# Performance work log

Measured on AMD Instinct MI355X. Metric: run time of the kernel, lower is better.

Reference implementation:

```python
import jax, jax.numpy as jnp
import numpy as np

EPS = 1e-5

def conv1x1(x, w, b):
    # x: [B,C,H,W], w: [O,C], b: [O]
    return jnp.einsum('oc,bchw->bohw', w, x) + b[None, :, None, None]

def mean_variance_norm(feat):
    # per-(batch,channel) stats over spatial dims; torch.var default is unbiased (ddof=1)
    b, c = feat.shape[:2]
    flat = feat.reshape(b, c, -1)
    mean = jnp.mean(flat, axis=2)[:, :, None, None]
    std = jnp.sqrt(jnp.var(flat, axis=2, ddof=1) + EPS)[:, :, None, None]
    return (feat - mean) / std

def setup_inputs() -> dict:
    key = jax.random.key(0)
    ks = jax.random.split(key, 10)
    B, C, H, W = 4, 256, 64, 64
    sc = 1.0 / np.sqrt(C)
    return {
        'content': jax.random.normal(ks[0], (B, C, H, W), jnp.float32),
        'style': jax.random.normal(ks[1], (B, C, H, W), jnp.float32),
        'content_key': jax.random.normal(ks[2], (B, C, H, W), jnp.float32),
        'style_key': jax.random.normal(ks[3], (B, C, H, W), jnp.float32),
        'f_w': jax.random.normal(ks[4], (C, C), jnp.float32) * sc,
        'f_b': jax.random.normal(ks[5], (C,), jnp.float32) * 0.01,
        'g_w': jax.random.normal(ks[6], (C, C), jnp.float32) * sc,
        'g_b': jax.random.normal(ks[7], (C,), jnp.float32) * 0.01,
        'h_w': jax.random.normal(ks[8], (C, C), jnp.float32) * sc,
        'h_b': jax.random.normal(ks[9], (C,), jnp.float32) * 0.01,
    }

def reference(content, style, content_key, style_key, f_w, f_b, g_w, g_b, h_w, h_b):
    Fq = conv1x1(content_key, f_w, f_b)   # [B,C,Hc,Wc]
    G = conv1x1(style_key, g_w, g_b)      # [B,C,Hs,Ws]
    Hv = conv1x1(style, h_w, h_b)         # [B,C,Hs,Ws]
    b, c, h, w = Fq.shape
    hw_c = h * w
    hw_s = G.shape[2] * G.shape[3]
    Fm = Fq.reshape(b, c, hw_c).transpose(0, 2, 1)       # [B,Nq,C]
    Gm = G.reshape(b, c, hw_s)                            # [B,C,Nk]
    style_flat = Hv.reshape(b, c, hw_s).transpose(0, 2, 1)  # [B,Nk,C]
    S = jax.nn.softmax(jnp.einsum('bqc,bck->bqk', Fm, Gm), axis=-1)  # [B,Nq,Nk]
    mean = jnp.einsum('bqk,bkc->bqc', S, style_flat)
    second = jnp.einsum('bqk,bkc->bqc', S, style_flat ** 2)
    std = jnp.sqrt(jax.nn.relu(second - mean ** 2))
    mean = mean.reshape(b, h, w, c).transpose(0, 3, 1, 2)
    std = std.reshape(b, h, w, c).transpose(0, 3, 1, 2)
    return std * mean_variance_norm(content) + mean
```

## Files before the change

kernel.cpp:

```cpp
#include <hip/hip_runtime.h>
#include <math.h>

#define NSP 4096
#define CD  256

typedef _Float16 half8 __attribute__((ext_vector_type(8)));
typedef _Float16 half4v __attribute__((ext_vector_type(4)));
typedef float f32x4 __attribute__((ext_vector_type(4)));
typedef unsigned int u32;

#define VMCNT(n) asm volatile("s_waitcnt vmcnt(" #n ")" ::: "memory")
#define LGKM0    asm volatile("s_waitcnt lgkmcnt(0)" ::: "memory")

__device__ __forceinline__ void gl16(const void* g, void* l) {
    __builtin_amdgcn_global_load_lds((const __attribute__((address_space(1))) u32*)g,
                                     (__attribute__((address_space(3))) u32*)l, 16, 0, 0);
}

template<int MODE>
__global__ __launch_bounds__(256, 2) void conv_kernel(
    const float* __restrict__ W, const float* __restrict__ bias,
    const float* __restrict__ Xall, _Float16* __restrict__ Yh, _Float16* __restrict__ Yl)
{
    const int b = blockIdx.z;
    const float* X = Xall + (size_t)b * CD * NSP;
    _Float16* Yhb = Yh + (size_t)b * CD * NSP;
    _Float16* Ylb = Yl + (size_t)b * CD * NSP;
    __shared__ float Ws[8][128];
    __shared__ float Xs[8][128];
    const int t = threadIdx.x;
    const int tx = t & 15, ty = t >> 4;
    const int m0 = blockIdx.y * 128, n0 = blockIdx.x * 128;
    float acc[8][8];
#pragma unroll
    for (int i = 0; i < 8; ++i)
#pragma unroll
        for (int j = 0; j < 8; ++j) acc[i][j] = 0.f;

    for (int k0 = 0; k0 < CD; k0 += 8) {
        __syncthreads();
        {
            int m = t >> 1, k = (t & 1) * 4;
            float4 wv = *reinterpret_cast<const float4*>(&W[(size_t)(m0 + m) * CD + k0 + k]);
            Ws[k + 0][m] = wv.x; Ws[k + 1][m] = wv.y; Ws[k + 2][m] = wv.z; Ws[k + 3][m] = wv.w;
        }
        {
            int k = t >> 5, n = (t & 31) * 4;
            *reinterpret_cast<float4*>(&Xs[k][n]) =
                *reinterpret_cast<const float4*>(&X[(size_t)(k0 + k) * NSP + n0 + n]);
        }
        __syncthreads();
#pragma unroll
        for (int k = 0; k < 8; ++k) {
            float a[8], bb[8];
            float4 a0 = *reinterpret_cast<const float4*>(&Ws[k][ty * 8]);
            float4 a1 = *reinterpret_cast<const float4*>(&Ws[k][ty * 8 + 4]);
            float4 b0 = *reinterpret_cast<const float4*>(&Xs[k][tx * 4]);
            float4 b1 = *reinterpret_cast<const float4*>(&Xs[k][64 + tx * 4]);
            a[0]=a0.x; a[1]=a0.y; a[2]=a0.z; a[3]=a0.w;
            a[4]=a1.x; a[5]=a1.y; a[6]=a1.z; a[7]=a1.w;
            bb[0]=b0.x; bb[1]=b0.y; bb[2]=b0.z; bb[3]=b0.w;
            bb[4]=b1.x; bb[5]=b1.y; bb[6]=b1.z; bb[7]=b1.w;
#pragma unroll
            for (int i = 0; i < 8; ++i)
#pragma unroll
                for (int j = 0; j < 8; ++j) acc[i][j] = fmaf(a[i], bb[j], acc[i][j]);
        }
    }
    float bv[8];
#pragma unroll
    for (int i = 0; i < 8; ++i) bv[i] = bias[m0 + ty * 8 + i];

    if (MODE == 0) {
#pragma unroll
        for (int jj = 0; jj < 8; ++jj) {
            int n = n0 + ((jj < 4) ? (tx * 4 + jj) : (64 + tx * 4 + (jj - 4)));
            half4v h0, h1, l0, l1;
#pragma unroll
            for (int i = 0; i < 4; ++i) {
                float y0 = acc[i][jj] + bv[i];
                _Float16 hh0 = (_Float16)y0; h0[i] = hh0; l0[i] = (_Float16)(y0 - (float)hh0);
                float y1 = acc[i + 4][jj] + bv[i + 4];
                _Float16 hh1 = (_Float16)y1; h1[i] = hh1; l1[i] = (_Float16)(y1 - (float)hh1);
            }
            size_t off = (size_t)n * CD + m0 + ty * 8;
            *reinterpret_cast<half4v*>(&Yhb[off])     = h0;
            *reinterpret_cast<half4v*>(&Yhb[off + 4]) = h1;
            *reinterpret_cast<half4v*>(&Ylb[off])     = l0;
            *reinterpret_cast<half4v*>(&Ylb[off + 4]) = l1;
        }
    } else if (MODE == 1) {
#pragma unroll
        for (int jj = 0; jj < 8; ++jj) {
            int n = n0 + ((jj < 4) ? (tx * 4 + jj) : (64 + tx * 4 + (jj - 4)));
            int tile = n >> 5, key = n & 31;
            int g = (m0 + ty * 8) >> 3;
            size_t base = (size_t)tile * 8192 + (size_t)key * 256
                        + ((((g * 16)) ^ ((key & 7) << 4)) >> 1);
            half4v h0, h1, l0, l1;
#pragma unroll
            for (int i = 0; i < 4; ++i) {
                float y0 = acc[i][jj] + bv[i];
                _Float16 hh0 = (_Float16)y0; h0[i] = hh0; l0[i] = (_Float16)(y0 - (float)hh0);
                float y1 = acc[i + 4][jj] + bv[i + 4];
                _Float16 hh1 = (_Float16)y1; h1[i] = hh1; l1[i] = (_Float16)(y1 - (float)hh1);
            }
            *reinterpret_cast<half4v*>(&Yhb[base])     = h0;
            *reinterpret_cast<half4v*>(&Yhb[base + 4]) = h1;
            *reinterpret_cast<half4v*>(&Ylb[base])     = l0;
            *reinterpret_cast<half4v*>(&Ylb[base + 4]) = l1;
        }
    } else {
#pragma unroll
        for (int i = 0; i < 8; ++i) {
            int ch = m0 + ty * 8 + i;
#pragma unroll
            for (int grp = 0; grp < 2; ++grp) {
                int n = n0 + grp * 64 + tx * 4;
                int tile = n >> 5, kin = n & 31;
                half4v hv, lv;
#pragma unroll
                for (int j = 0; j < 4; ++j) {
                    float y = acc[i][grp * 4 + j] + bv[i];
                    _Float16 hh = (_Float16)y; hv[j] = hh; lv[j] = (_Float16)(y - (float)hh);
                }
                size_t base = (size_t)tile * 8192 + (size_t)ch * 32
                            + ((((kin * 2)) ^ ((ch & 3) << 4)) >> 1);
                *reinterpret_cast<half4v*>(&Yhb[base]) = hv;
                *reinterpret_cast<half4v*>(&Ylb[base]) = lv;
            }
        }
    }
}

#define KB_OFF 0
#define VB_OFF 65536
#define PB_OFF 131072
#define RM_OFF 139264
#define RS_OFF 139776
#define SMEM_BYTES 140800

__global__ __launch_bounds__(512, 2) void attn_kernel(
    const _Float16* __restrict__ Qh_g, const _Float16* __restrict__ Ql_g,
    const _Float16* __restrict__ Kh_g, const _Float16* __restrict__ Kl_g,
    const _Float16* __restrict__ Vh_g, const _Float16* __restrict__ Vl_g,
    float* __restrict__ Mout, float* __restrict__ Sout)
{
    extern __shared__ char smem[];
    const int tid = threadIdx.x;
    const int lane = tid & 63;
    const int w = tid >> 6;
    const int g4 = lane >> 4;
    const int l15 = lane & 15;
    const int qf = w & 3;
    const int kf = w >> 2;

    const int bid = blockIdx.x;
    const int b = (bid & 7) >> 1;
    const int qb = ((bid >> 3) << 1) | (bid & 1);
    const int q0 = qb * 64;

    const size_t bNC = (size_t)b * NSP * CD;
    const _Float16* Qhb = Qh_g + bNC;
    const _Float16* Qlb = Ql_g + bNC;
    const _Float16* Khb = Kh_g + bNC;
    const _Float16* Klb = Kl_g + bNC;
    const _Float16* Vhb = Vh_g + bNC;
    const _Float16* Vlb = Vl_g + bNC;

    const int qrow = q0 + qf * 16 + l15;
    half8 qh[8], ql[8];
#pragma unroll
    for (int ks = 0; ks < 8; ++ks) {
        qh[ks] = *reinterpret_cast<const half8*>(Qhb + (size_t)qrow * CD + ks * 32 + g4 * 8);
        ql[ks] = *reinterpret_cast<const half8*>(Qlb + (size_t)qrow * CD + ks * 32 + g4 * 8);
    }

    auto stageK = [&](int t, int buf) {
        const _Float16* sh = Khb + (size_t)t * 8192 + w * 1024 + lane * 8;
        const _Float16* sl = Klb + (size_t)t * 8192 + w * 1024 + lane * 8;
        char* d = smem + KB_OFF + buf * 32768 + w * 2048;
        gl16(sh,       d);
        gl16(sh + 512, d + 1024);
        gl16(sl,       d + 16384);
        gl16(sl + 512, d + 16384 + 1024);
    };
    auto stageV = [&](int t, int buf) {
        const _Float16* sh = Vhb + (size_t)t * 8192 + w * 1024 + lane * 8;
        const _Float16* sl = Vlb + (size_t)t * 8192 + w * 1024 + lane * 8;
        char* d = smem + VB_OFF + buf * 32768 + w * 2048;
        gl16(sh,       d);
        gl16(sh + 512, d + 1024);
        gl16(sl,       d + 16384);
        gl16(sl + 512, d + 16384 + 1024);
    };

    stageK(0, 0); stageV(0, 0); stageK(1, 1); stageV(1, 1);

    f32x4 accM[2][4], accS[2][4];
#pragma unroll
    for (int m = 0; m < 2; ++m)
#pragma unroll
        for (int nf = 0; nf < 4; ++nf) {
            accM[m][nf] = (f32x4){0.f, 0.f, 0.f, 0.f};
            accS[m][nf] = (f32x4){0.f, 0.f, 0.f, 0.f};
        }
    float mrun = -3.0e38f, lrun = 0.f;

    const int key = kf * 16 + l15;
    const int ksw = (key & 7) << 4;

    for (int t = 0; t < 128; ++t) {
        const int buf = t & 1;

        if (t < 127) { VMCNT(12); } else { VMCNT(4); }
        LGKM0;
        __builtin_amdgcn_s_barrier();
        __builtin_amdgcn_sched_barrier(0);

        if (t > 0) {
            const float* rs = (const float*)(smem + RS_OFF + ((t + 1) & 1) * 512);
            lrun += rs[lane] + rs[64 + lane];
        }

        const char* krow = smem + KB_OFF + buf * 32768 + key * 512;
        f32x4 s = (f32x4){0.f, 0.f, 0.f, 0.f};
        __builtin_amdgcn_s_setprio(1);
#pragma unroll
        for (int ks = 0; ks < 8; ++ks) {
            int off = ((ks * 4 + g4) * 16) ^ ksw;
            half8 bh = *reinterpret_cast<const half8*>(krow + off);
            half8 bl = *reinterpret_cast<const half8*>(krow + 16384 + off);
            s = __builtin_amdgcn_mfma_f32_16x16x32_f16(qh[ks], bh, s, 0, 0, 0);
            s = __builtin_amdgcn_mfma_f32_16x16x32_f16(qh[ks], bl, s, 0, 0, 0);
            s = __builtin_amdgcn_mfma_f32_16x16x32_f16(ql[ks], bh, s, 0, 0, 0);
        }
        __builtin_amdgcn_s_setprio(0);

        f32x4 rmax = s;
#pragma unroll
        for (int mk = 1; mk <= 8; mk <<= 1)
#pragma unroll
            for (int e = 0; e < 4; ++e) rmax[e] = fmaxf(rmax[e], __shfl_xor(rmax[e], mk));
        if (l15 == 0)
            *reinterpret_cast<f32x4*>(smem + RM_OFF + kf * 256 + (qf * 16 + g4 * 4) * 4) = rmax;

        LGKM0;
        __builtin_amdgcn_s_barrier();
        __builtin_amdgcn_sched_barrier(0);

        if (t + 2 < 128) stageK(t + 2, buf);

        const float* rmf = (const float*)(smem + RM_OFF);
        float rm01 = fmaxf(rmf[lane], rmf[64 + lane]);
        bool upd = rm01 > mrun + 6.f;
        float sc = upd ? __expf(mrun - rm01) : 1.f;
        if (upd) mrun = rm01;
        lrun *= sc;

        float psum[4];
#pragma unroll
        for (int e = 0; e < 4; ++e) {
            int q_e = qf * 16 + g4 * 4 + e;
            float m_e = __shfl(mrun, q_e);
            float p = __expf(s[e] - m_e);
            _Float16 hp = (_Float16)p;
            *reinterpret_cast<_Float16*>(smem + PB_OFF + q_e * 128 + ((key * 2) ^ ((q_e & 7) << 4))) = hp;
            psum[e] = (float)hp;
        }
#pragma unroll
        for (int mk = 1; mk <= 8; mk <<= 1)
#pragma unroll
            for (int e = 0; e < 4; ++e) psum[e] += __shfl_xor(psum[e], mk);
        if (l15 == 0) {
            f32x4 ps4 = {psum[0], psum[1], psum[2], psum[3]};
            *reinterpret_cast<f32x4*>(smem + RS_OFF + buf * 512 + kf * 256 + (qf * 16 + g4 * 4) * 4) = ps4;
        }

        if (__ballot(sc < 1.f)) {
#pragma unroll
            for (int nf = 0; nf < 4; ++nf) {
                float scn = __shfl(sc, nf * 16 + l15);
#pragma unroll
                for (int m = 0; m < 2; ++m)
#pragma unroll
                    for (int e = 0; e < 4; ++e) { accM[m][nf][e] *= scn; accS[m][nf][e] *= scn; }
            }
        }

        if (t < 126) { VMCNT(12); } else if (t == 126) { VMCNT(8); } else { VMCNT(0); }
        LGKM0;
        __builtin_amdgcn_s_barrier();
        __builtin_amdgcn_sched_barrier(0);

        half8 pb[4];
#pragma unroll
        for (int nf = 0; nf < 4; ++nf) {
            int q = nf * 16 + l15;
            pb[nf] = *reinterpret_cast<const half8*>(smem + PB_OFF + q * 128 + ((g4 * 16) ^ ((q & 7) << 4)));
        }
        const char* vb = smem + VB_OFF + buf * 32768;
        __builtin_amdgcn_s_setprio(1);
#pragma unroll
        for (int m = 0; m < 2; ++m) {
            int ch = w * 32 + m * 16 + l15;
            const char* vrow = vb + ch * 64;
            int voff = (g4 * 16) ^ ((ch & 3) << 4);
            half8 vh8 = *reinterpret_cast<const half8*>(vrow + voff);
            half8 vl8 = *reinterpret_cast<const half8*>(vrow + 16384 + voff);
            half8 wh8, wl8;
#pragma unroll
            for (int e = 0; e < 8; ++e) {
                float v = (float)vh8[e] + (float)vl8[e];
                float wv = v * v;
                _Float16 hh = (_Float16)wv;
                wh8[e] = hh; wl8[e] = (_Float16)(wv - (float)hh);
            }
#pragma unroll
            for (int nf = 0; nf < 4; ++nf) {
                accM[m][nf] = __builtin_amdgcn_mfma_f32_16x16x32_f16(vh8, pb[nf], accM[m][nf], 0, 0, 0);
                accM[m][nf] = __builtin_amdgcn_mfma_f32_16x16x32_f16(vl8, pb[nf], accM[m][nf], 0, 0, 0);
                accS[m][nf] = __builtin_amdgcn_mfma_f32_16x16x32_f16(wh8, pb[nf], accS[m][nf], 0, 0, 0);
                accS[m][nf] = __builtin_amdgcn_mfma_f32_16x16x32_f16(wl8, pb[nf], accS[m][nf], 0, 0, 0);
            }
        }
        __builtin_amdgcn_s_setprio(0);
        __builtin_amdgcn_sched_barrier(0);
        LGKM0;
        if (t + 2 < 128) stageV(t + 2, buf);
    }

    {
        const float* rs = (const float*)(smem + RS_OFF + 512);
        lrun += rs[lane] + rs[64 + lane];
    }
    float inv = 1.f / lrun;
    float linv[4];
#pragma unroll
    for (int nf = 0; nf < 4; ++nf) linv[nf] = __shfl(inv, nf * 16 + l15);

#pragma unroll
    for (int m = 0; m < 2; ++m)
#pragma unroll
        for (int nf = 0; nf < 4; ++nf) {
            int qg = q0 + nf * 16 + l15;
#pragma unroll
            for (int e = 0; e < 4; ++e) {
                int ch = w * 32 + m * 16 + g4 * 4 + e;
                float mean = accM[m][nf][e] * linv[nf];
                float sec  = accS[m][nf][e] * linv[nf];
                float var = sec - mean * mean;
                float sd = sqrtf(fmaxf(var, 0.f));
                size_t off = ((size_t)b * CD + ch) * NSP + qg;
                Mout[off] = mean;
                Sout[off] = sd;
            }
        }
}

__global__ __launch_bounds__(256) void mvn_kernel(
    const float* __restrict__ content, const float* __restrict__ Mn,
    const float* __restrict__ Sd, float* __restrict__ out)
{
    __shared__ float redS[4], redSS[4];
    const int t = threadIdx.x;
    const size_t base = (size_t)blockIdx.x * NSP;
    const float4* x4 = reinterpret_cast<const float4*>(content + base);
    float s = 0.f, ss = 0.f;
    float4 xv[4];
#pragma unroll
    for (int i = 0; i < 4; ++i) {
        float4 v = x4[i * 256 + t];
        xv[i] = v;
        s  += v.x + v.y + v.z + v.w;
        ss += v.x * v.x + v.y * v.y + v.z * v.z + v.w * v.w;
    }
#pragma unroll
    for (int mk = 1; mk < 64; mk <<= 1) { s += __shfl_xor(s, mk); ss += __shfl_xor(ss, mk); }
    if ((t & 63) == 0) { redS[t >> 6] = s; redSS[t >> 6] = ss; }
    __syncthreads();
    float tot   = redS[0] + redS[1] + redS[2] + redS[3];
    float totss = redSS[0] + redSS[1] + redSS[2] + redSS[3];
    float mu  = tot * (1.f / 4096.f);
    float var = (totss - 4096.f * mu * mu) * (1.f / 4095.f);
    float rstd = 1.f / sqrtf(var + 1e-5f);
    const float4* m4 = reinterpret_cast<const float4*>(Mn + base);
    const float4* s4 = reinterpret_cast<const float4*>(Sd + base);
    float4* o4 = reinterpret_cast<float4*>(out + base);
#pragma unroll
    for (int i = 0; i < 4; ++i) {
        float4 mv = m4[i * 256 + t];
        float4 sv = s4[i * 256 + t];
        float4 v  = xv[i];
        float4 o;
        o.x = sv.x * ((v.x - mu) * rstd) + mv.x;
        o.y = sv.y * ((v.y - mu) * rstd) + mv.y;
        o.z = sv.z * ((v.z - mu) * rstd) + mv.z;
        o.w = sv.w * ((v.w - mu) * rstd) + mv.w;
        o4[i * 256 + t] = o;
    }
}

extern "C" void kernel_launch(void* const* d_in, const int* in_sizes, int n_in,
                              void* d_out, int out_size, void* d_ws, size_t ws_size,
                              hipStream_t stream)
{
    const float* content     = (const float*)d_in[0];
    const float* style       = (const float*)d_in[1];
    const float* content_key = (const float*)d_in[2];
    const float* style_key   = (const float*)d_in[3];
    const float* f_w = (const float*)d_in[4];
    const float* f_b = (const float*)d_in[5];
    const float* g_w = (const float*)d_in[6];
    const float* g_b = (const float*)d_in[7];
    const float* h_w = (const float*)d_in[8];
    const float* h_b = (const float*)d_in[9];
    float* out = (float*)d_out;

    const size_t TS = (size_t)4 * NSP * CD;
    _Float16* ws16 = (_Float16*)d_ws;
    _Float16* Qh = ws16;
    _Float16* Ql = ws16 + TS;
    _Float16* Kh = ws16 + 2 * TS;
    _Float16* Kl = ws16 + 3 * TS;
    _Float16* Vh = ws16 + 4 * TS;
    _Float16* Vl = ws16 + 5 * TS;
    float* Mn = (float*)(ws16 + 6 * TS);
    float* Sd = Mn + TS;

    dim3 cgrid(32, 2, 4);
    conv_kernel<0><<<cgrid, 256, 0, stream>>>(f_w, f_b, content_key, Qh, Ql);
    conv_kernel<1><<<cgrid, 256, 0, stream>>>(g_w, g_b, style_key, Kh, Kl);
    conv_kernel<2><<<cgrid, 256, 0, stream>>>(h_w, h_b, style, Vh, Vl);
    attn_kernel<<<dim3(256), 512, SMEM_BYTES, stream>>>(Qh, Ql, Kh, Kl, Vh, Vl, Mn, Sd);
    mvn_kernel<<<dim3(1024), 256, 0, stream>>>(content, Mn, Sd, out);
}
```

Measured before the change: 647.5 us.

## Interleave V hi/lo tiles, fold log2e into Q, compute row sums via MFMA

Several changes land together. The conv kernel now uses a K-step of 16. Q is pre-scaled by log2e so the softmax can use exp2 directly. V hi and lo halves are packed into one interleaved, swizzled tile, so each staged V tile is one contiguous 32KB load. In the attention loop, the cross-lane shuffle reduction and shared-memory exchange of P row sums are replaced by an MFMA against a vector of ones, and the V loads and V-squared preparation move ahead of the QK stage. The rescale threshold rises from 6 to 8 and the wait counts are retuned, which adds extra MFMA work and register pressure in exchange for fewer shuffles and fewer barriers' worth of shared traffic.

New measurement: 571.8 us. -11.7%, faster.

```diff
diff --git a/kernel.cpp b/kernel.cpp
--- a/kernel.cpp
+++ b/kernel.cpp
@@ -3,6 +3,7 @@
 
 #define NSP 4096
 #define CD  256
+#define LOG2E 1.44269504f
 
 typedef _Float16 half8 __attribute__((ext_vector_type(8)));
 typedef _Float16 half4v __attribute__((ext_vector_type(4)));
@@ -24,10 +25,10 @@
 {
     const int b = blockIdx.z;
     const float* X = Xall + (size_t)b * CD * NSP;
-    _Float16* Yhb = Yh + (size_t)b * CD * NSP;
-    _Float16* Ylb = Yl + (size_t)b * CD * NSP;
-    __shared__ float Ws[8][128];
-    __shared__ float Xs[8][128];
+    _Float16* Yhb = Yh + (size_t)b * CD * NSP * (MODE == 2 ? 2 : 1);
+    _Float16* Ylb = (MODE == 2) ? nullptr : Yl + (size_t)b * CD * NSP;
+    __shared__ float Ws[16][128];
+    __shared__ float Xs[16][128];
     const int t = threadIdx.x;
     const int tx = t & 15, ty = t >> 4;
     const int m0 = blockIdx.y * 128, n0 = blockIdx.x * 128;
@@ -37,21 +38,25 @@
 #pragma unroll
         for (int j = 0; j < 8; ++j) acc[i][j] = 0.f;
 
-    for (int k0 = 0; k0 < CD; k0 += 8) {
+    for (int k0 = 0; k0 < CD; k0 += 16) {
         __syncthreads();
         {
-            int m = t >> 1, k = (t & 1) * 4;
-            float4 wv = *reinterpret_cast<const float4*>(&W[(size_t)(m0 + m) * CD + k0 + k]);
-            Ws[k + 0][m] = wv.x; Ws[k + 1][m] = wv.y; Ws[k + 2][m] = wv.z; Ws[k + 3][m] = wv.w;
+            int m = t >> 1, k = (t & 1) * 8;
+            float4 w0 = *reinterpret_cast<const float4*>(&W[(size_t)(m0 + m) * CD + k0 + k]);
+            float4 w1 = *reinterpret_cast<const float4*>(&W[(size_t)(m0 + m) * CD + k0 + k + 4]);
+            Ws[k + 0][m] = w0.x; Ws[k + 1][m] = w0.y; Ws[k + 2][m] = w0.z; Ws[k + 3][m] = w0.w;
+            Ws[k + 4][m] = w1.x; Ws[k + 5][m] = w1.y; Ws[k + 6][m] = w1.z; Ws[k + 7][m] = w1.w;
         }
         {
-            int k = t >> 5, n = (t & 31) * 4;
+            int k = t >> 4, n = (t & 15) * 8;
             *reinterpret_cast<float4*>(&Xs[k][n]) =
                 *reinterpret_cast<const float4*>(&X[(size_t)(k0 + k) * NSP + n0 + n]);
+            *reinterpret_cast<float4*>(&Xs[k][n + 4]) =
+                *reinterpret_cast<const float4*>(&X[(size_t)(k0 + k) * NSP + n0 + n + 4]);
         }
         __syncthreads();
 #pragma unroll
-        for (int k = 0; k < 8; ++k) {
+        for (int k = 0; k < 16; ++k) {
             float a[8], bb[8];
             float4 a0 = *reinterpret_cast<const float4*>(&Ws[k][ty * 8]);
             float4 a1 = *reinterpret_cast<const float4*>(&Ws[k][ty * 8 + 4]);
@@ -78,9 +83,9 @@
             half4v h0, h1, l0, l1;
 #pragma unroll
             for (int i = 0; i < 4; ++i) {
-                float y0 = acc[i][jj] + bv[i];
+                float y0 = (acc[i][jj] + bv[i]) * LOG2E;
                 _Float16 hh0 = (_Float16)y0; h0[i] = hh0; l0[i] = (_Float16)(y0 - (float)hh0);
-                float y1 = acc[i + 4][jj] + bv[i + 4];
+                float y1 = (acc[i + 4][jj] + bv[i + 4]) * LOG2E;
                 _Float16 hh1 = (_Float16)y1; h1[i] = hh1; l1[i] = (_Float16)(y1 - (float)hh1);
             }
             size_t off = (size_t)n * CD + m0 + ty * 8;
@@ -114,20 +119,23 @@
 #pragma unroll
         for (int i = 0; i < 8; ++i) {
             int ch = m0 + ty * 8 + i;
+            int sw = (ch & 7) << 4;
 #pragma unroll
             for (int grp = 0; grp < 2; ++grp) {
                 int n = n0 + grp * 64 + tx * 4;
                 int tile = n >> 5, kin = n & 31;
+                int g4 = kin >> 3, pos0 = kin & 7;
                 half4v hv, lv;
 #pragma unroll
                 for (int j = 0; j < 4; ++j) {
                     float y = acc[i][grp * 4 + j] + bv[i];
                     _Float16 hh = (_Float16)y; hv[j] = hh; lv[j] = (_Float16)(y - (float)hh);
                 }
-                size_t base = (size_t)tile * 8192 + (size_t)ch * 32
-                            + ((((kin * 2)) ^ ((ch & 3) << 4)) >> 1);
-                *reinterpret_cast<half4v*>(&Yhb[base]) = hv;
-                *reinterpret_cast<half4v*>(&Ylb[base]) = lv;
+                size_t rowb = (size_t)tile * 16384 + (size_t)ch * 64;
+                int bh = (g4 * 16 + pos0 * 2) ^ sw;
+                int bl = (64 + g4 * 16 + pos0 * 2) ^ sw;
+                *reinterpret_cast<half4v*>(&Yhb[rowb + (bh >> 1)]) = hv;
+                *reinterpret_cast<half4v*>(&Yhb[rowb + (bl >> 1)]) = lv;
             }
         }
     }
@@ -137,13 +145,12 @@
 #define VB_OFF 65536
 #define PB_OFF 131072
 #define RM_OFF 139264
-#define RS_OFF 139776
-#define SMEM_BYTES 140800
+#define SMEM_BYTES 139776
 
 __global__ __launch_bounds__(512, 2) void attn_kernel(
     const _Float16* __restrict__ Qh_g, const _Float16* __restrict__ Ql_g,
     const _Float16* __restrict__ Kh_g, const _Float16* __restrict__ Kl_g,
-    const _Float16* __restrict__ Vh_g, const _Float16* __restrict__ Vl_g,
+    const _Float16* __restrict__ Vhl_g,
     float* __restrict__ Mout, float* __restrict__ Sout)
 {
     extern __shared__ char smem[];
@@ -165,8 +172,7 @@
     const _Float16* Qlb = Ql_g + bNC;
     const _Float16* Khb = Kh_g + bNC;
     const _Float16* Klb = Kl_g + bNC;
-    const _Float16* Vhb = Vh_g + bNC;
-    const _Float16* Vlb = Vl_g + bNC;
+    const _Float16* Vb  = Vhl_g + bNC * 2;
 
     const int qrow = q0 + qf * 16 + l15;
     half8 qh[8], ql[8];
@@ -186,13 +192,12 @@
         gl16(sl + 512, d + 16384 + 1024);
     };
     auto stageV = [&](int t, int buf) {
-        const _Float16* sh = Vhb + (size_t)t * 8192 + w * 1024 + lane * 8;
-        const _Float16* sl = Vlb + (size_t)t * 8192 + w * 1024 + lane * 8;
-        char* d = smem + VB_OFF + buf * 32768 + w * 2048;
-        gl16(sh,       d);
-        gl16(sh + 512, d + 1024);
-        gl16(sl,       d + 16384);
-        gl16(sl + 512, d + 16384 + 1024);
+        const _Float16* s = Vb + (size_t)t * 16384 + w * 2048 + lane * 8;
+        char* d = smem + VB_OFF + buf * 32768 + w * 4096;
+        gl16(s,        d);
+        gl16(s + 512,  d + 1024);
+        gl16(s + 1024, d + 2048);
+        gl16(s + 1536, d + 3072);
     };
 
     stageK(0, 0); stageV(0, 0); stageK(1, 1); stageV(1, 1);
@@ -207,20 +212,39 @@
         }
     float mrun = -3.0e38f, lrun = 0.f;
 
+    half8 ones8;
+#pragma unroll
+    for (int e = 0; e < 8; ++e) ones8[e] = (_Float16)1.f;
+
     const int key = kf * 16 + l15;
     const int ksw = (key & 7) << 4;
 
     for (int t = 0; t < 128; ++t) {
         const int buf = t & 1;
 
-        if (t < 127) { VMCNT(12); } else { VMCNT(4); }
+        if (t < 127) { VMCNT(8); } else { VMCNT(0); }
         LGKM0;
         __builtin_amdgcn_s_barrier();
         __builtin_amdgcn_sched_barrier(0);
 
-        if (t > 0) {
-            const float* rs = (const float*)(smem + RS_OFF + ((t + 1) & 1) * 512);
-            lrun += rs[lane] + rs[64 + lane];
+        half8 vh8A[2], vl8A[2], wh8A[2], wl8A[2];
+#pragma unroll
+        for (int m = 0; m < 2; ++m) {
+            int ch = w * 32 + m * 16 + l15;
+            const char* vrow = smem + VB_OFF + buf * 32768 + ch * 128;
+            int sw = (ch & 7) << 4;
+            half8 vh8 = *reinterpret_cast<const half8*>(vrow + ((g4 * 16) ^ sw));
+            half8 vl8 = *reinterpret_cast<const half8*>(vrow + ((64 + g4 * 16) ^ sw));
+            vh8A[m] = vh8; vl8A[m] = vl8;
+            half8 wh8, wl8;
+#pragma unroll
+            for (int e = 0; e < 8; ++e) {
+                float v = (float)vh8[e] + (float)vl8[e];
+                float wv = v * v;
+                _Float16 hh = (_Float16)wv;
+                wh8[e] = hh; wl8[e] = (_Float16)(wv - (float)hh);
+            }
+            wh8A[m] = wh8; wl8A[m] = wl8;
         }
 
         const char* krow = smem + KB_OFF + buf * 32768 + key * 512;
@@ -253,28 +277,17 @@
 
         const float* rmf = (const float*)(smem + RM_OFF);
         float rm01 = fmaxf(rmf[lane], rmf[64 + lane]);
-        bool upd = rm01 > mrun + 6.f;
-        float sc = upd ? __expf(mrun - rm01) : 1.f;
+        bool upd = rm01 > mrun + 8.f;
+        float sc = upd ? __builtin_amdgcn_exp2f(mrun - rm01) : 1.f;
         if (upd) mrun = rm01;
-        lrun *= sc;
-
-        float psum[4];
+
 #pragma unroll
         for (int e = 0; e < 4; ++e) {
             int q_e = qf * 16 + g4 * 4 + e;
             float m_e = __shfl(mrun, q_e);
-            float p = __expf(s[e] - m_e);
+            float p = __builtin_amdgcn_exp2f(s[e] - m_e);
             _Float16 hp = (_Float16)p;
             *reinterpret_cast<_Float16*>(smem + PB_OFF + q_e * 128 + ((key * 2) ^ ((q_e & 7) << 4))) = hp;
-            psum[e] = (float)hp;
-        }
-#pragma unroll
-        for (int mk = 1; mk <= 8; mk <<= 1)
-#pragma unroll
-            for (int e = 0; e < 4; ++e) psum[e] += __shfl_xor(psum[e], mk);
-        if (l15 == 0) {
-            f32x4 ps4 = {psum[0], psum[1], psum[2], psum[3]};
-            *reinterpret_cast<f32x4*>(smem + RS_OFF + buf * 512 + kf * 256 + (qf * 16 + g4 * 4) * 4) = ps4;
         }
 
         if (__ballot(sc < 1.f)) {
@@ -288,7 +301,6 @@
             }
         }
 
-        if (t < 126) { VMCNT(12); } else if (t == 126) { VMCNT(8); } else { VMCNT(0); }
         LGKM0;
         __builtin_amdgcn_s_barrier();
         __builtin_amdgcn_sched_barrier(0);
@@ -299,41 +311,33 @@
             int q = nf * 16 + l15;
             pb[nf] = *reinterpret_cast<const half8*>(smem + PB_OFF + q * 128 + ((g4 * 16) ^ ((q & 7) << 4)));
         }
-        const char* vb = smem + VB_OFF + buf * 32768;
+        f32x4 po[4];
+#pragma unroll
+        for (int nf = 0; nf < 4; ++nf) po[nf] = (f32x4){0.f, 0.f, 0.f, 0.f};
         __builtin_amdgcn_s_setprio(1);
 #pragma unroll
+        for (int nf = 0; nf < 4; ++nf)
+            po[nf] = __builtin_amdgcn_mfma_f32_16x16x32_f16(ones8, pb[nf], po[nf], 0, 0, 0);
+#pragma unroll
         for (int m = 0; m < 2; ++m) {
-            int ch = w * 32 + m * 16 + l15;
-            const char* vrow = vb + ch * 64;
-            int voff = (g4 * 16) ^ ((ch & 3) << 4);
-            half8 vh8 = *reinterpret_cast<const half8*>(vrow + voff);
-            half8 vl8 = *reinterpret_cast<const half8*>(vrow + 16384 + voff);
-            half8 wh8, wl8;
-#pragma unroll
-            for (int e = 0; e < 8; ++e) {
-                float v = (float)vh8[e] + (float)vl8[e];
-                float wv = v * v;
-                _Float16 hh = (_Float16)wv;
-                wh8[e] = hh; wl8[e] = (_Float16)(wv - (float)hh);
-            }
 #pragma unroll
             for (int nf = 0; nf < 4; ++nf) {
-                accM[m][nf] = __builtin_amdgcn_mfma_f32_16x16x32_f16(vh8, pb[nf], accM[m][nf], 0, 0, 0);
-                accM[m][nf] = __builtin_amdgcn_mfma_f32_16x16x32_f16(vl8, pb[nf], accM[m][nf], 0, 0, 0);
-                accS[m][nf] = __builtin_amdgcn_mfma_f32_16x16x32_f16(wh8, pb[nf], accS[m][nf], 0, 0, 0);
-                accS[m][nf] = __builtin_amdgcn_mfma_f32_16x16x32_f16(wl8, pb[nf], accS[m][nf], 0, 0, 0);
+                accM[m][nf] = __builtin_amdgcn_mfma_f32_16x16x32_f16(vh8A[m], pb[nf], accM[m][nf], 0, 0, 0);
+                accM[m][nf] = __builtin_amdgcn_mfma_f32_16x16x32_f16(vl8A[m], pb[nf], accM[m][nf], 0, 0, 0);
+                accS[m][nf] = __builtin_amdgcn_mfma_f32_16x16x32_f16(wh8A[m], pb[nf], accS[m][nf], 0, 0, 0);
+                accS[m][nf] = __builtin_amdgcn_mfma_f32_16x16x32_f16(wl8A[m], pb[nf], accS[m][nf], 0, 0, 0);
             }
         }
         __builtin_amdgcn_s_setprio(0);
+
+        float rsum = (g4 == 0) ? po[0][0] : (g4 == 1) ? po[1][0] : (g4 == 2) ? po[2][0] : po[3][0];
+        lrun = lrun * sc + rsum;
+
         __builtin_amdgcn_sched_barrier(0);
         LGKM0;
         if (t + 2 < 128) stageV(t + 2, buf);
     }
 
-    {
-        const float* rs = (const float*)(smem + RS_OFF + 512);
-        lrun += rs[lane] + rs[64 + lane];
-    }
     float inv = 1.f / lrun;
     float linv[4];
 #pragma unroll
@@ -419,19 +423,18 @@
 
     const size_t TS = (size_t)4 * NSP * CD;
     _Float16* ws16 = (_Float16*)d_ws;
-    _Float16* Qh = ws16;
-    _Float16* Ql = ws16 + TS;
-    _Float16* Kh = ws16 + 2 * TS;
-    _Float16* Kl = ws16 + 3 * TS;
-    _Float16* Vh = ws16 + 4 * TS;
-    _Float16* Vl = ws16 + 5 * TS;
+    _Float16* Qh  = ws16;
+    _Float16* Ql  = ws16 + TS;
+    _Float16* Kh  = ws16 + 2 * TS;
+    _Float16* Kl  = ws16 + 3 * TS;
+    _Float16* Vhl = ws16 + 4 * TS;
     float* Mn = (float*)(ws16 + 6 * TS);
     float* Sd = Mn + TS;
 
     dim3 cgrid(32, 2, 4);
     conv_kernel<0><<<cgrid, 256, 0, stream>>>(f_w, f_b, content_key, Qh, Ql);
     conv_kernel<1><<<cgrid, 256, 0, stream>>>(g_w, g_b, style_key, Kh, Kl);
-    conv_kernel<2><<<cgrid, 256, 0, stream>>>(h_w, h_b, style, Vh, Vl);
-    attn_kernel<<<dim3(256), 512, SMEM_BYTES, stream>>>(Qh, Ql, Kh, Kl, Vh, Vl, Mn, Sd);
+    conv_kernel<2><<<cgrid, 256, 0, stream>>>(h_w, h_b, style, Vhl, Vhl);
+    attn_kernel<<<dim3(256), 512, SMEM_BYTES, stream>>>(Qh, Ql, Kh, Kl, Vhl, Mn, Sd);
     mvn_kernel<<<dim3(1024), 256, 0, stream>>>(content, Mn, Sd, out);
 }
```
